# Kernel optimization log

Measured on AMD Instinct MI355X. Metric: run time of the kernel, lower is better.

Reference implementation:

```python
import jax, jax.numpy as jnp
import numpy as np

BN_EPS = 1e-5


def setup_inputs() -> dict:
    key = jax.random.key(0)
    ks = jax.random.split(key, 12)
    N, K, C_IN, C_OUT = 50000, 16, 128, 128
    C2 = 2 * C_OUT
    return {
        "features": jax.random.normal(ks[0], (N, C_IN), dtype=jnp.float32),
        "neighbor_idx": jax.random.randint(ks[1], (N, K), 0, N, dtype=jnp.int64),
        "W1": jax.random.normal(ks[2], (C_IN, C2), dtype=jnp.float32) * 0.05,
        "b1": jax.random.normal(ks[3], (C2,), dtype=jnp.float32) * 0.05,
        "gamma": jax.random.uniform(ks[4], (C2,), dtype=jnp.float32, minval=0.5, maxval=1.5),
        "beta": jax.random.normal(ks[5], (C2,), dtype=jnp.float32) * 0.05,
        "run_mean": jax.random.normal(ks[6], (C2,), dtype=jnp.float32) * 0.05,
        "run_var": jax.random.uniform(ks[7], (C2,), dtype=jnp.float32, minval=0.5, maxval=1.5),
        "Ws": jax.random.normal(ks[8], (C2, C2), dtype=jnp.float32) * 0.05,
        "Wm": jax.random.normal(ks[9], (C2, C_OUT), dtype=jnp.float32) * 0.05,
        "bm": jax.random.normal(ks[10], (C_OUT,), dtype=jnp.float32) * 0.05,
    }


def reference(features, neighbor_idx, W1, b1, gamma, beta, run_mean, run_var, Ws, Wm, bm):
    # mlp1: Linear + ReLU (no BN)
    x = jax.nn.relu(features @ W1 + b1)                     # (N, 2C)
    # gather_neighbour: irregular index_select
    g = x[neighbor_idx]                                     # (N, k, 2C)
    # BatchNorm1d over channel dim (inference semantics, running stats)
    inv = gamma * jax.lax.rsqrt(run_var + BN_EPS)
    g = (g - run_mean) * inv + beta                         # (N, k, 2C)
    # AttentivePooling: per-neighbor score linear (no bias), softmax over k
    scores = jax.nn.softmax(g @ Ws, axis=1)                 # (N, k, 2C)
    feat = jnp.sum(scores * g, axis=1)                      # (N, 2C)
    return feat @ Wm + bm                                   # (N, C_out)
```

## Files before the change

### kernel.cpp

```cpp
#include <hip/hip_runtime.h>
#include <cstddef>

#define C_IN  128
#define C2    256
#define C_OUT 128
#define KNBR  16
#define PTS   32

typedef unsigned short u16;
typedef __attribute__((ext_vector_type(8))) short bf16x8;
typedef __attribute__((ext_vector_type(8))) unsigned short u16x8;
typedef __attribute__((ext_vector_type(4))) float f32x4;

__device__ __forceinline__ float bf2f(u16 h) {
    return __uint_as_float(((unsigned int)h) << 16);
}
__device__ __forceinline__ u16 f2bf(float x) {
    unsigned int u = __float_as_uint(x);
    return (u16)((u + 0x7fffu + ((u >> 16) & 1u)) >> 16);
}

__global__ void prep_k(const float* __restrict__ W1, const float* __restrict__ Ws,
                       const float* __restrict__ Wm, u16* __restrict__ W1t,
                       u16* __restrict__ Wst, u16* __restrict__ Wmt)
{
    const int n = blockIdx.x, t = threadIdx.x;
    if (blockIdx.y == 0) {
        if (t < 128) W1t[n * 128 + t] = f2bf(W1[t * 256 + n]);
    } else if (blockIdx.y == 1) {
        Wst[n * 256 + t] = f2bf(Ws[t * 256 + n]);
    } else {
        if (n < 128) Wmt[n * 256 + t] = f2bf(Wm[t * 128 + n]);
    }
}


__global__ __launch_bounds__(256)
void mlp_k(const float* __restrict__ F, const u16* __restrict__ W1t,
           const u16* __restrict__ Wst,
           const float* __restrict__ bias, const float* __restrict__ gamma,
           const float* __restrict__ beta, const float* __restrict__ mean,
           const float* __restrict__ var,
           u16* __restrict__ packed, int N)
{
    __shared__ u16 As[64][136];
    __shared__ u16 Bs[128][72];
    __shared__ u16 xs[64][264];

    const int tid = threadIdx.x;
    const int w = tid >> 6, l = tid & 63, q = l >> 4, r = l & 15;
    const int wm = w & 1, wn = w >> 1;
    const int m0 = blockIdx.x * 64;

    #pragma unroll
    for (int i = 0; i < 8; i++) {
        int idx = tid + i * 256;
        int row = idx >> 5, c4 = (idx & 31) * 4;
        int gm = m0 + row;
        float4 v = make_float4(0.f, 0.f, 0.f, 0.f);
        if (gm < N) v = *(const float4*)(F + (size_t)gm * C_IN + c4);
        ushort4 h;
        h.x = f2bf(v.x); h.y = f2bf(v.y); h.z = f2bf(v.z); h.w = f2bf(v.w);
        *(ushort4*)&As[row][c4] = h;
    }

    #pragma unroll
    for (int nh = 0; nh < 2; nh++) {
        f32x4 acc[2][4] = {};
        #pragma unroll 1
        for (int k0 = 0; k0 < C_IN; k0 += 64) {
            __syncthreads();
            #pragma unroll
            for (int i = 0; i < 4; i++) {
                int idx = tid + i * 256;
                int row = idx >> 3, g = (idx & 7) * 8;
                *(uint4*)&Bs[row][g] = *(const uint4*)(
                    W1t + (size_t)(nh * 128 + row) * C_IN + k0 + g);
            }
            __syncthreads();
            #pragma unroll
            for (int h = 0; h < 2; h++) {
                bf16x8 af[2], bfr[4];
                #pragma unroll
                for (int i = 0; i < 2; i++)
                    af[i] = *(const bf16x8*)&As[wm * 32 + i * 16 + r][k0 + h * 32 + q * 8];
                #pragma unroll
                for (int j = 0; j < 4; j++)
                    bfr[j] = *(const bf16x8*)&Bs[wn * 64 + j * 16 + r][h * 32 + q * 8];
                #pragma unroll
                for (int i = 0; i < 2; i++)
                    #pragma unroll
                    for (int j = 0; j < 4; j++)
                        acc[i][j] = __builtin_amdgcn_mfma_f32_16x16x32_bf16(
                            af[i], bfr[j], acc[i][j], 0, 0, 0);
            }
        }
        #pragma unroll
        for (int j = 0; j < 4; j++) {
            const int ch = nh * 128 + wn * 64 + j * 16 + r;
            const float bi = bias[ch], be = beta[ch], mu = mean[ch];
            const float iv = gamma[ch] * rsqrtf(var[ch] + 1e-5f);
            #pragma unroll
            for (int i = 0; i < 2; i++) {
                const int mb = wm * 32 + i * 16 + q * 4;
                #pragma unroll
                for (int p = 0; p < 4; p++) {
                    float x = fmaxf(acc[i][j][p] + bi, 0.f);
                    x = (x - mu) * iv + be;
                    xs[mb + p][ch] = f2bf(x);
                }
            }
        }
    }
    __syncthreads();

    #pragma unroll
    for (int nh = 0; nh < 2; nh++) {
        f32x4 acc[2][4] = {};
        #pragma unroll 1
        for (int k0 = 0; k0 < C2; k0 += 64) {
            __syncthreads();
            #pragma unroll
            for (int i = 0; i < 4; i++) {
                int idx = tid + i * 256;
                int row = idx >> 3, g = (idx & 7) * 8;
                *(uint4*)&Bs[row][g] = *(const uint4*)(
                    Wst + (size_t)(nh * 128 + row) * C2 + k0 + g);
            }
            __syncthreads();
            #pragma unroll
            for (int h = 0; h < 2; h++) {
                bf16x8 af[2], bfr[4];
                #pragma unroll
                for (int i = 0; i < 2; i++)
                    af[i] = *(const bf16x8*)&xs[wm * 32 + i * 16 + r][k0 + h * 32 + q * 8];
                #pragma unroll
                for (int j = 0; j < 4; j++)
                    bfr[j] = *(const bf16x8*)&Bs[wn * 64 + j * 16 + r][h * 32 + q * 8];
                #pragma unroll
                for (int i = 0; i < 2; i++)
                    #pragma unroll
                    for (int j = 0; j < 4; j++)
                        acc[i][j] = __builtin_amdgcn_mfma_f32_16x16x32_bf16(
                            af[i], bfr[j], acc[i][j], 0, 0, 0);
            }
        }
        __syncthreads();
        #pragma unroll
        for (int j = 0; j < 4; j++) {
            const int chl = wn * 64 + j * 16 + r;
            #pragma unroll
            for (int i = 0; i < 2; i++) {
                const int mb = wm * 32 + i * 16 + q * 4;
                #pragma unroll
                for (int p = 0; p < 4; p++)
                    As[mb + p][chl] = f2bf(__expf(acc[i][j][p]));
            }
        }
        __syncthreads();
        #pragma unroll
        for (int i = 0; i < 8; i++) {
            int idx = tid + i * 256;
            int row = idx >> 5, slot = idx & 31;
            int c0 = slot * 4;
            if (m0 + row < N) {
                ushort4 e  = *(const ushort4*)&As[row][c0];
                ushort4 xv = *(const ushort4*)&xs[row][nh * 128 + c0];
                uint4 qv;
                qv.x = (unsigned)e.x | ((unsigned)xv.x << 16);
                qv.y = (unsigned)e.y | ((unsigned)xv.y << 16);
                qv.z = (unsigned)e.z | ((unsigned)xv.z << 16);
                qv.w = (unsigned)e.w | ((unsigned)xv.w << 16);
                *(uint4*)(packed + (size_t)(m0 + row) * 512 + nh * 256 + slot * 8) = qv;
            }
        }
    }
}

__global__ __launch_bounds__(256)
void gather_out_k(const u16* __restrict__ packed, const int* __restrict__ nidx,
                  const u16* __restrict__ Bt, const float* __restrict__ bias,
                  float* __restrict__ Cf, int N)
{
    __shared__ int rows[PTS * KNBR];
    __shared__ u16 Bs[128][72];
    __shared__ __align__(16) u16 fsm[PTS * 264];

    const int tid = threadIdx.x;
    const int w = tid >> 6, l = tid & 63, q = l >> 4, r = l & 15;
    const int m0 = blockIdx.x * PTS;

    #pragma unroll
    for (int i = 0; i < 2; i++) {
        int idx = tid + i * 256;
        int n = m0 + (idx >> 4);
        rows[idx] = (n < N) ? nidx[n * KNBR + (idx & 15)] : 0;
    }
    __syncthreads();

    #pragma unroll 1
    for (int ip = 0; ip < 8; ip++) {
        const int pl = w * 8 + ip;
        u16x8 v[KNBR];
        #pragma unroll
        for (int k = 0; k < KNBR; k++)
            v[k] = *(const u16x8*)(packed + (size_t)rows[pl * KNBR + k] * 512 + l * 8);
        float num[4] = {0.f, 0.f, 0.f, 0.f};
        float den[4] = {0.f, 0.f, 0.f, 0.f};
        #pragma unroll
        for (int k = 0; k < KNBR; k++) {
            #pragma unroll
            for (int c = 0; c < 4; c++) {
                float e = bf2f((u16)v[k][2 * c]);
                float x = bf2f((u16)v[k][2 * c + 1]);
                den[c] += e;
                num[c] = fmaf(e, x, num[c]);
            }
        }
        ushort4 o;
        o.x = f2bf(num[0] / den[0]); o.y = f2bf(num[1] / den[1]);
        o.z = f2bf(num[2] / den[2]); o.w = f2bf(num[3] / den[3]);
        *(ushort4*)&fsm[pl * 264 + l * 4] = o;
    }
    __syncthreads();

    const int wm = w & 1, wn = w >> 1;
    f32x4 acc[4] = {};

    #pragma unroll 1
    for (int k0 = 0; k0 < C2; k0 += 64) {
        __syncthreads();
        #pragma unroll
        for (int i = 0; i < 4; i++) {
            int idx = tid + i * 256;
            int row = idx >> 3, g = (idx & 7) * 8;
            *(uint4*)&Bs[row][g] = *(const uint4*)(
                Bt + (size_t)row * C2 + k0 + g);
        }
        __syncthreads();
        #pragma unroll
        for (int h = 0; h < 2; h++) {
            bf16x8 af, bfr[4];
            af = *(const bf16x8*)&fsm[(wm * 16 + r) * 264 + k0 + h * 32 + q * 8];
            #pragma unroll
            for (int j = 0; j < 4; j++)
                bfr[j] = *(const bf16x8*)&Bs[wn * 64 + j * 16 + r][h * 32 + q * 8];
            #pragma unroll
            for (int j = 0; j < 4; j++)
                acc[j] = __builtin_amdgcn_mfma_f32_16x16x32_bf16(
                    af, bfr[j], acc[j], 0, 0, 0);
        }
    }
    __syncthreads();

    float* STF = (float*)fsm;
    #pragma unroll
    for (int j = 0; j < 4; j++) {
        const int ch = wn * 64 + j * 16 + r;
        const float bo = bias[ch];
        const int mb = wm * 16 + q * 4;
        #pragma unroll
        for (int p = 0; p < 4; p++)
            STF[(mb + p) * 132 + ch] = acc[j][p] + bo;
    }
    __syncthreads();
    #pragma unroll
    for (int i = 0; i < 4; i++) {
        int idx = tid + i * 256;
        int row = idx >> 5, c4 = (idx & 31) * 4;
        if (m0 + row < N)
            *(float4*)(Cf + (size_t)(m0 + row) * C_OUT + c4) =
                *(const float4*)&STF[row * 132 + c4];
    }
}

extern "C" void kernel_launch(void* const* d_in, const int* in_sizes, int n_in,
                              void* d_out, int out_size, void* d_ws, size_t ws_size,
                              hipStream_t stream)
{
    const float* features = (const float*)d_in[0];
    const int*   nidx     = (const int*)d_in[1];
    const float* W1       = (const float*)d_in[2];
    const float* b1       = (const float*)d_in[3];
    const float* gamma    = (const float*)d_in[4];
    const float* beta     = (const float*)d_in[5];
    const float* mean     = (const float*)d_in[6];
    const float* var      = (const float*)d_in[7];
    const float* Ws       = (const float*)d_in[8];
    const float* Wm       = (const float*)d_in[9];
    const float* bm       = (const float*)d_in[10];
    float* out = (float*)d_out;

    const int N = in_sizes[0] / C_IN;

    u16* packed = (u16*)d_ws;
    u16* W1t    = packed + (size_t)N * 512;
    u16* Wst    = W1t + 256 * 128;
    u16* Wmt    = Wst + 256 * 256;

    prep_k<<<dim3(256, 3), 256, 0, stream>>>(W1, Ws, Wm, W1t, Wst, Wmt);

    const int MT = (N + 63) / 64;
    const int GT = (N + PTS - 1) / PTS;

    mlp_k<<<MT, 256, 0, stream>>>(features, W1t, Wst, b1, gamma, beta,
                                  mean, var, packed, N);
    gather_out_k<<<GT, 256, 0, stream>>>(packed, nidx, Wmt, bm, out, N);
}
```

Baseline: 255.0 us.

## Load GEMM weight fragments directly from global memory, dropping LDS staging

In all three GEMM stages, weight fragments are now read straight from global memory into registers instead of being staged through a shared-memory B tile. This removes the Bs buffer and the per-k-step barriers, and the k loops are fully unrolled. Less LDS per block plus the new occupancy hints in launch_bounds are meant to let more blocks run per CU. The cost is redundant global/L2 traffic, since each wave reloads weight rows that were previously shared across the block, and possibly higher register pressure.

New measurement: 491.9 us. +92.9%, slower.

```diff
diff --git a/kernel.cpp b/kernel.cpp
--- a/kernel.cpp
+++ b/kernel.cpp
@@ -35,7 +35,7 @@
 }
 
 
-__global__ __launch_bounds__(256)
+__global__ __launch_bounds__(256, 3)
 void mlp_k(const float* __restrict__ F, const u16* __restrict__ W1t,
            const u16* __restrict__ Wst,
            const float* __restrict__ bias, const float* __restrict__ gamma,
@@ -44,7 +44,6 @@
            u16* __restrict__ packed, int N)
 {
     __shared__ u16 As[64][136];
-    __shared__ u16 Bs[128][72];
     __shared__ u16 xs[64][264];
 
     const int tid = threadIdx.x;
@@ -63,21 +62,13 @@
         h.x = f2bf(v.x); h.y = f2bf(v.y); h.z = f2bf(v.z); h.w = f2bf(v.w);
         *(ushort4*)&As[row][c4] = h;
     }
+    __syncthreads();
 
     #pragma unroll
     for (int nh = 0; nh < 2; nh++) {
         f32x4 acc[2][4] = {};
-        #pragma unroll 1
+        #pragma unroll
         for (int k0 = 0; k0 < C_IN; k0 += 64) {
-            __syncthreads();
-            #pragma unroll
-            for (int i = 0; i < 4; i++) {
-                int idx = tid + i * 256;
-                int row = idx >> 3, g = (idx & 7) * 8;
-                *(uint4*)&Bs[row][g] = *(const uint4*)(
-                    W1t + (size_t)(nh * 128 + row) * C_IN + k0 + g);
-            }
-            __syncthreads();
             #pragma unroll
             for (int h = 0; h < 2; h++) {
                 bf16x8 af[2], bfr[4];
@@ -86,7 +77,9 @@
                     af[i] = *(const bf16x8*)&As[wm * 32 + i * 16 + r][k0 + h * 32 + q * 8];
                 #pragma unroll
                 for (int j = 0; j < 4; j++)
-                    bfr[j] = *(const bf16x8*)&Bs[wn * 64 + j * 16 + r][h * 32 + q * 8];
+                    bfr[j] = *(const bf16x8*)(W1t +
+                        (size_t)(nh * 128 + wn * 64 + j * 16 + r) * C_IN +
+                        k0 + h * 32 + q * 8);
                 #pragma unroll
                 for (int i = 0; i < 2; i++)
                     #pragma unroll
@@ -117,17 +110,8 @@
     #pragma unroll
     for (int nh = 0; nh < 2; nh++) {
         f32x4 acc[2][4] = {};
-        #pragma unroll 1
+        #pragma unroll
         for (int k0 = 0; k0 < C2; k0 += 64) {
-            __syncthreads();
-            #pragma unroll
-            for (int i = 0; i < 4; i++) {
-                int idx = tid + i * 256;
-                int row = idx >> 3, g = (idx & 7) * 8;
-                *(uint4*)&Bs[row][g] = *(const uint4*)(
-                    Wst + (size_t)(nh * 128 + row) * C2 + k0 + g);
-            }
-            __syncthreads();
             #pragma unroll
             for (int h = 0; h < 2; h++) {
                 bf16x8 af[2], bfr[4];
@@ -136,7 +120,9 @@
                     af[i] = *(const bf16x8*)&xs[wm * 32 + i * 16 + r][k0 + h * 32 + q * 8];
                 #pragma unroll
                 for (int j = 0; j < 4; j++)
-                    bfr[j] = *(const bf16x8*)&Bs[wn * 64 + j * 16 + r][h * 32 + q * 8];
+                    bfr[j] = *(const bf16x8*)(Wst +
+                        (size_t)(nh * 128 + wn * 64 + j * 16 + r) * C2 +
+                        k0 + h * 32 + q * 8);
                 #pragma unroll
                 for (int i = 0; i < 2; i++)
                     #pragma unroll
@@ -145,7 +131,7 @@
                             af[i], bfr[j], acc[i][j], 0, 0, 0);
             }
         }
-        __syncthreads();
+        if (nh == 1) __syncthreads();
         #pragma unroll
         for (int j = 0; j < 4; j++) {
             const int chl = wn * 64 + j * 16 + r;
@@ -177,13 +163,12 @@
     }
 }
 
-__global__ __launch_bounds__(256)
+__global__ __launch_bounds__(256, 6)
 void gather_out_k(const u16* __restrict__ packed, const int* __restrict__ nidx,
                   const u16* __restrict__ Bt, const float* __restrict__ bias,
                   float* __restrict__ Cf, int N)
 {
     __shared__ int rows[PTS * KNBR];
-    __shared__ u16 Bs[128][72];
     __shared__ __align__(16) u16 fsm[PTS * 264];
 
     const int tid = threadIdx.x;
@@ -227,24 +212,16 @@
     const int wm = w & 1, wn = w >> 1;
     f32x4 acc[4] = {};
 
-    #pragma unroll 1
+    #pragma unroll
     for (int k0 = 0; k0 < C2; k0 += 64) {
-        __syncthreads();
-        #pragma unroll
-        for (int i = 0; i < 4; i++) {
-            int idx = tid + i * 256;
-            int row = idx >> 3, g = (idx & 7) * 8;
-            *(uint4*)&Bs[row][g] = *(const uint4*)(
-                Bt + (size_t)row * C2 + k0 + g);
-        }
-        __syncthreads();
         #pragma unroll
         for (int h = 0; h < 2; h++) {
             bf16x8 af, bfr[4];
             af = *(const bf16x8*)&fsm[(wm * 16 + r) * 264 + k0 + h * 32 + q * 8];
             #pragma unroll
             for (int j = 0; j < 4; j++)
-                bfr[j] = *(const bf16x8*)&Bs[wn * 64 + j * 16 + r][h * 32 + q * 8];
+                bfr[j] = *(const bf16x8*)(Bt +
+                    (size_t)(wn * 64 + j * 16 + r) * C2 + k0 + h * 32 + q * 8);
             #pragma unroll
             for (int j = 0; j < 4; j++)
                 acc[j] = __builtin_amdgcn_mfma_f32_16x16x32_bf16(
```
